# Performance work log

Hardware: AMD Instinct MI355X
Metric: run time of the kernel (lower is better)

The kernel has to match this reference:

```python
import jax, jax.numpy as jnp
import numpy as np

B = 4096
D = 64  # emb_dim, hardcoded in UserEmb/ItemEmb


def setup_inputs() -> dict:
    key = jax.random.key(0)
    ks = jax.random.split(key, 26)
    n = lambda k, shape, s=1.0: jax.random.normal(k, shape, dtype=jnp.float32) * s
    inp = {
        'user_emb': jax.random.randint(ks[0], (B, 4), 0, 6, dtype=jnp.int32),
        'item_emb': jax.random.randint(ks[1], (B, 10242), 0, 2, dtype=jnp.int32),
        'edge_emb': jnp.zeros((B,), dtype=jnp.int32),  # edges_emb has num_embeddings=1
        # UserEmb params
        'gender_tab': n(ks[2], (98, D)),
        'age_tab': n(ks[3], (7, D)),
        'occ_tab': n(ks[4], (21, D)),
        'area_tab': n(ks[5], (3402, D)),
        'user_W': n(ks[6], (4 * D, D), 0.05),  # stored [in,out]
        'user_b': n(ks[7], (D,), 0.05),
        # ItemEmb params
        'rate_tab': n(ks[8], (6, D)),
        'genre_W': n(ks[9], (25, D), 0.05),
        'director_W': n(ks[10], (2186, D), 0.02),
        'actor_W': n(ks[11], (8030, D), 0.01),
        'item_W': n(ks[12], (4 * D, D), 0.05),
        'item_b': n(ks[13], (D,), 0.05),
        # GLNFeat params (torch: randn * 0.5)
        'edges_tab': n(ks[14], (1, D)),
        'uu_w': n(ks[15], (D,), 0.5),
        'ui_w': n(ks[16], (D,), 0.5),
        'iu_w': n(ks[17], (D,), 0.5),
        'ii_w': n(ks[18], (D,), 0.5),
        'edge_W': n(ks[19], (D, D), 0.5),
        'uu_W1': n(ks[20], (D, D), 0.5),
        'ui_W1': n(ks[21], (D, D), 0.5),
        'iu_W1': n(ks[22], (D, D), 0.5),
        'ii_W1': n(ks[23], (D, D), 0.5),
    }
    return inp


def _lrelu(v):
    return jnp.where(v >= 0, v, 0.01 * v)  # nn.LeakyReLU default slope


def reference(user_emb, item_emb, edge_emb, gender_tab, age_tab, occ_tab, area_tab,
              user_W, user_b, rate_tab, genre_W, director_W, actor_W, item_W, item_b,
              edges_tab, uu_w, ui_w, iu_w, ii_w, edge_W, uu_W1, ui_W1, iu_W1, ii_W1):
    a = 0.12
    b = 0.12
    # UserEmb
    u_cat = jnp.concatenate([gender_tab[user_emb[:, 0]], age_tab[user_emb[:, 1]],
                             occ_tab[user_emb[:, 2]], area_tab[user_emb[:, 3]]], axis=1)
    x = (u_cat @ user_W + user_b) * a  # [B, D]
    # ItemEmb: multi-hot fields projected then mean-normalized by count
    genre = item_emb[:, 1:26].astype(jnp.float32)
    director = item_emb[:, 26:2212].astype(jnp.float32)
    actor = item_emb[:, 2212:10242].astype(jnp.float32)
    ge = (genre @ genre_W) / jnp.sum(genre, 1, keepdims=True)
    de = (director @ director_W) / jnp.sum(director, 1, keepdims=True)
    ae = (actor @ actor_W) / jnp.sum(actor, 1, keepdims=True)
    i_cat = jnp.concatenate([rate_tab[item_emb[:, 0]], ge, de, ae], axis=1)
    y = (i_cat @ item_W + item_b) * a  # [B, D]
    edge = edges_tab[edge_emb] * b  # [B, D]

    def outer_mm(u, v, M):
        # stop_gradient(outer(u, v) @ M) == u[:,None] * (v @ M), avoids [B,B]
        return jax.lax.stop_gradient(u[:, None] * (v @ M))

    xe = x * edge
    ye = y * edge
    x_xx = xe @ uu_w      # [B]
    x_xy_x = xe @ ui_w
    x_xy_y = ye @ ui_w
    t1 = outer_mm(x_xx, x_xx, x)
    t2 = outer_mm(x_xy_x, x_xy_y, y)
    x_buy = (_lrelu(t1 @ uu_W1) + _lrelu(t2 @ ui_W1)) / 2
    y_yy = ye @ ii_w
    y_yx_y = ye @ iu_w
    y_yx_x = xe @ iu_w
    t3 = outer_mm(y_yy, y_yy, y)
    t4 = outer_mm(y_yx_y, y_yx_x, x)
    y_buy = (_lrelu(t3 @ ii_W1) + _lrelu(t4 @ iu_W1)) / 2
    new = _lrelu(edge @ edge_W)
    return ((x_buy + x) / 2, (y_buy + y) / 2, (new + edge) / 2)
```

## Files before the change

### kernel.cpp

```cpp
#include <hip/hip_runtime.h>
#include <cstddef>

constexpr int BATCH = 4096;
constexpr int ITEM_COLS = 10242;
constexpr int FBTK = 10304;

constexpr int R_GENDER = 0;
constexpr int R_AGE    = 98;
constexpr int R_OCC    = 105;
constexpr int R_AREA   = 126;
constexpr int R_RATE   = 3528;
constexpr int R_FU     = 3534;

constexpr size_t OFF_FU  = 0;
constexpr size_t OFF_NEW = OFF_FU + (size_t)R_FU * 64;
constexpr size_t OFF_FBT = OFF_NEW + 64;
constexpr size_t OFF_X   = OFF_FBT + (size_t)64 * FBTK / 2;
constexpr size_t OFF_Y   = OFF_X + (size_t)BATCH * 64;
constexpr size_t OFF_P   = OFF_Y + (size_t)BATCH * 64;
constexpr size_t OFF_C   = OFF_P + 9ull * BATCH * 64;
constexpr size_t OFF_SP  = OFF_C + 9ull * BATCH;
constexpr size_t OFF_PB  = OFF_SP + 256ull * 256;
constexpr size_t OFF_SC  = OFF_PB + 4ull * 64;

__device__ const int ASTART[9] = {1, 25, 1113, 2209, 3545, 4881, 6225, 7561, 8897};
__device__ const int VSTART[9] = {1, 26, 1119, 2212, 3550, 4888, 6227, 7565, 8903};
__device__ const int VEND[9]   = {26, 1119, 2212, 3550, 4888, 6227, 7565, 8903, 10242};

typedef __attribute__((ext_vector_type(8))) short bf16x8;
typedef __attribute__((ext_vector_type(4))) float f32x4;

__device__ __forceinline__ float lrelu(float v) { return v >= 0.0f ? v : 0.01f * v; }

__device__ __forceinline__ short bf_trunc(float f) {
    return (short)(__builtin_bit_cast(unsigned, f) >> 16);
}
__device__ __forceinline__ unsigned bf_rne_pair(float lo, float hi) {
    unsigned ul = __builtin_bit_cast(unsigned, lo);
    unsigned uh = __builtin_bit_cast(unsigned, hi);
    ul += 0x7fffu + ((ul >> 16) & 1u);
    uh += 0x7fffu + ((uh >> 16) & 1u);
    return (ul >> 16) | (uh & 0xffff0000u);
}

__global__ __launch_bounds__(256) void k_fuseA(
        const float* __restrict__ gender_tab, const float* __restrict__ age_tab,
        const float* __restrict__ occ_tab, const float* __restrict__ area_tab,
        const float* __restrict__ user_W, const float* __restrict__ rate_tab,
        const float* __restrict__ item_W, const float* __restrict__ edges_tab,
        const float* __restrict__ edge_W, float* __restrict__ Fu, float* __restrict__ NEWt) {
    int t = threadIdx.x;
    int n = t & 63;
    int rb = __builtin_amdgcn_readfirstlane(t >> 6);
    int r = blockIdx.x * 4 + rb;
    if (r > R_FU) return;
    if (r == R_FU) {
        float acc = 0.0f;
#pragma unroll
        for (int k = 0; k < 64; ++k)
            acc = fmaf(edges_tab[k] * 0.12f, edge_W[k * 64 + n], acc);
        NEWt[n] = lrelu(acc);
        return;
    }
    const float* src;
    const float* W;
    if (r < R_AGE)       { src = gender_tab + (size_t)r * 64;            W = user_W;            }
    else if (r < R_OCC)  { src = age_tab    + (size_t)(r - R_AGE) * 64;  W = user_W + 64 * 64;  }
    else if (r < R_AREA) { src = occ_tab    + (size_t)(r - R_OCC) * 64;  W = user_W + 128 * 64; }
    else if (r < R_RATE) { src = area_tab   + (size_t)(r - R_AREA) * 64; W = user_W + 192 * 64; }
    else                 { src = rate_tab   + (size_t)(r - R_RATE) * 64; W = item_W;            }
    float acc = 0.0f;
#pragma unroll
    for (int k = 0; k < 64; ++k)
        acc = fmaf(src[k], W[k * 64 + n], acc);
    Fu[(size_t)r * 64 + n] = acc;
}

__global__ __launch_bounds__(256) void k_fuseT(
        const float* __restrict__ genre_W, const float* __restrict__ director_W,
        const float* __restrict__ actor_W, const float* __restrict__ item_W,
        short* __restrict__ Fbt) {
    const int t = threadIdx.x;
    const int KT0 = blockIdx.x * 64;
    const int n = t & 63;
    const int rb = __builtin_amdgcn_readfirstlane(t >> 6);
    __shared__ float T[64 * 65];
    for (int rl = 0; rl < 16; ++rl) {
        int r = rl * 4 + rb;
        int KT = KT0 + r;
        float acc = 0.0f;
        if (KT < 10241) {
            const float* src;
            const float* W;
            if (KT < 25)        { src = genre_W    + (size_t)KT * 64;          W = item_W + 64 * 64;  }
            else if (KT < 2211) { src = director_W + (size_t)(KT - 25) * 64;   W = item_W + 128 * 64; }
            else                { src = actor_W    + (size_t)(KT - 2211) * 64; W = item_W + 192 * 64; }
#pragma unroll
            for (int k = 0; k < 64; ++k)
                acc = fmaf(src[k], W[k * 64 + n], acc);
        }
        T[r * 65 + n] = acc;
    }
    __syncthreads();
    int n2 = t >> 2, sg = t & 3;
    unsigned dw[8];
#pragma unroll
    for (int d = 0; d < 8; ++d)
        dw[d] = bf_rne_pair(T[(sg * 16 + 2 * d) * 65 + n2], T[(sg * 16 + 2 * d + 1) * 65 + n2]);
    uint4* dst = (uint4*)(Fbt + (size_t)n2 * FBTK + KT0 + sg * 16);
    dst[0] = make_uint4(dw[0], dw[1], dw[2], dw[3]);
    dst[1] = make_uint4(dw[4], dw[5], dw[6], dw[7]);
}

__global__ __launch_bounds__(256) void k_item(const int* __restrict__ item,
                                              const short* __restrict__ Fbt,
                                              float* __restrict__ P, float* __restrict__ C) {
    const int ch = blockIdx.y;
    const int astart = ASTART[ch], vs = VSTART[ch], ve = VEND[ch];
    const int len = ve - astart;
    const int KT0 = astart - 1;
    const int m0 = blockIdx.x * 64;
    const int t = threadIdx.x;
    const int lane = t & 63;
    const int w = __builtin_amdgcn_readfirstlane(t >> 6);
    const int q = lane >> 4, r16 = lane & 15;

    __shared__ short As[64 * 136];
    __shared__ short Bs[64 * 136];

    f32x4 acc[5];
#pragma unroll
    for (int s = 0; s < 5; ++s) acc[s] = (f32x4){0.f, 0.f, 0.f, 0.f};

    short o = (r16 == 0) ? (short)0x3f80 : (short)0;
    bf16x8 ones = {o, o, o, o, o, o, o, o};

    for (int kb = 0; kb < len; kb += 128) {
        __syncthreads();
        const int c0 = astart + kb;
        if (c0 >= vs && c0 + 128 <= ve) {
#pragma unroll
            for (int it = 0; it < 32; ++it) {
                int f = it * 256 + t;
                int r = f >> 7, cc = f & 127;
                int v = item[(size_t)(m0 + r) * ITEM_COLS + c0 + cc];
                As[r * 136 + cc] = bf_trunc((float)v);
            }
        } else {
#pragma unroll
            for (int it = 0; it < 32; ++it) {
                int f = it * 256 + t;
                int r = f >> 7, cc = f & 127;
                int c = c0 + cc;
                int v = (c >= vs && c < ve) ? item[(size_t)(m0 + r) * ITEM_COLS + c] : 0;
                As[r * 136 + cc] = bf_trunc((float)v);
            }
        }
        {
            int nB = t >> 2, pt = t & 3;
            const short* fb = Fbt + (size_t)nB * FBTK + KT0 + kb;
#pragma unroll
            for (int p = 0; p < 4; ++p) {
                int off = (p * 4 + pt) * 8;
                *(uint4*)(Bs + nB * 136 + off) = *(const uint4*)(fb + off);
            }
        }
        __syncthreads();
#pragma unroll
        for (int kt = 0; kt < 4; ++kt) {
            bf16x8 a = *(const bf16x8*)(As + (w * 16 + r16) * 136 + kt * 32 + q * 8);
#pragma unroll
            for (int s = 0; s < 4; ++s) {
                bf16x8 b = *(const bf16x8*)(Bs + (s * 16 + r16) * 136 + kt * 32 + q * 8);
                acc[s] = __builtin_amdgcn_mfma_f32_16x16x32_bf16(a, b, acc[s], 0, 0, 0);
            }
            acc[4] = __builtin_amdgcn_mfma_f32_16x16x32_bf16(a, ones, acc[4], 0, 0, 0);
        }
    }
    const size_t pb = (size_t)ch * BATCH + m0 + w * 16 + q * 4;
#pragma unroll
    for (int reg = 0; reg < 4; ++reg) {
        float* pr = P + (pb + reg) * 64 + r16;
        pr[0] = acc[0][reg];
        pr[16] = acc[1][reg];
        pr[32] = acc[2][reg];
        pr[48] = acc[3][reg];
    }
    if (r16 == 0) {
#pragma unroll
        for (int reg = 0; reg < 4; ++reg)
            C[(size_t)ch * BATCH + m0 + w * 16 + q * 4 + reg] = acc[4][reg];
    }
}

__device__ __forceinline__ float wred(float v) {
#pragma unroll
    for (int m = 1; m < 64; m <<= 1) v += __shfl_xor(v, m, 64);
    return v;
}

__global__ __launch_bounds__(256) void k_mid(const int* __restrict__ item, const int* __restrict__ edge_emb,
                                             const int* __restrict__ user_emb,
                                             const float* __restrict__ Fu, const float* __restrict__ user_b,
                                             const float* __restrict__ P, const float* __restrict__ C,
                                             const float* __restrict__ item_b, const float* __restrict__ edges_tab,
                                             const float* __restrict__ uu_w, const float* __restrict__ ui_w,
                                             const float* __restrict__ iu_w, const float* __restrict__ ii_w,
                                             float* __restrict__ X, float* __restrict__ Y,
                                             float* __restrict__ SC, float* __restrict__ SP) {
    const int t = threadIdx.x;
    const int n = t & 63;
    const int wv = __builtin_amdgcn_readfirstlane(t >> 6);
    const float uuw = uu_w[n], uiw = ui_w[n], iuw = iu_w[n], iiw = ii_w[n];
    const float ib = item_b[n], ub = user_b[n];
    const size_t cs = (size_t)BATCH * 64;
    float s1 = 0.0f, s2 = 0.0f, s3 = 0.0f, s4 = 0.0f;

    for (int i = 0; i < 4; ++i) {
        int b = blockIdx.x * 16 + wv * 4 + i;
        const int* ue = user_emb + (size_t)b * 4;
        float x = (Fu[(size_t)(R_GENDER + ue[0]) * 64 + n]
                 + Fu[(size_t)(R_AGE    + ue[1]) * 64 + n]
                 + Fu[(size_t)(R_OCC    + ue[2]) * 64 + n]
                 + Fu[(size_t)(R_AREA   + ue[3]) * 64 + n] + ub) * 0.12f;
        X[(size_t)b * 64 + n] = x;
        int ri = item[(size_t)b * ITEM_COLS];
        size_t base = (size_t)b * 64 + n;
        float sg = P[base];
        float sd = P[base + cs] + P[base + 2 * cs];
        float sa = P[base + 3 * cs] + P[base + 4 * cs] + P[base + 5 * cs]
                 + P[base + 6 * cs] + P[base + 7 * cs] + P[base + 8 * cs];
        float cg = C[b];
        float cd = C[BATCH + b] + C[2 * BATCH + b];
        float ca = C[3 * BATCH + b] + C[4 * BATCH + b] + C[5 * BATCH + b]
                 + C[6 * BATCH + b] + C[7 * BATCH + b] + C[8 * BATCH + b];
        float y = (Fu[(size_t)(R_RATE + ri) * 64 + n] + sg / cg + sd / cd + sa / ca + ib) * 0.12f;
        Y[(size_t)b * 64 + n] = y;
        float e = edges_tab[(size_t)edge_emb[b] * 64 + n] * 0.12f;
        float xe = x * e, ye = y * e;
        float r1 = wred(xe * uuw);
        float r2 = wred(xe * uiw);
        float r3 = wred(xe * iuw);
        float r4 = wred(ye * uiw);
        float r5 = wred(ye * iiw);
        float r6 = wred(ye * iuw);
        if (n == 0) {
            SC[b] = r1; SC[BATCH + b] = r2; SC[2 * BATCH + b] = r5; SC[3 * BATCH + b] = r6;
        }
        s1 = fmaf(r1, x, s1);
        s2 = fmaf(r4, y, s2);
        s3 = fmaf(r5, y, s3);
        s4 = fmaf(r3, x, s4);
    }
    __shared__ float sp[4][4][64];
    sp[wv][0][n] = s1; sp[wv][1][n] = s2; sp[wv][2][n] = s3; sp[wv][3][n] = s4;
    __syncthreads();
    int i2 = t >> 6;
    float v = sp[0][i2][n] + sp[1][i2][n] + sp[2][i2][n] + sp[3][i2][n];
    SP[(size_t)blockIdx.x * 256 + t] = v;
}

__global__ __launch_bounds__(1024) void k_red(const float* __restrict__ SP,
                                              const float* __restrict__ uu_W1, const float* __restrict__ ui_W1,
                                              const float* __restrict__ iu_W1, const float* __restrict__ ii_W1,
                                              float* __restrict__ PB) {
    int t = threadIdx.x;
    int sub = t >> 8, i = (t >> 6) & 3, n = t & 63;
    float s = 0.0f;
    for (int wb = sub * 64; wb < sub * 64 + 64; ++wb)
        s += SP[(size_t)wb * 256 + i * 64 + n];
    __shared__ float red[4][4][64];
    red[sub][i][n] = s;
    __syncthreads();
    float sv = red[0][i][n] + red[1][i][n] + red[2][i][n] + red[3][i][n];
    __shared__ float sl[4][64];
    if (t < 256) sl[i][n] = sv;
    __syncthreads();
    if (t < 256) {
        const float* W1 = (i == 0) ? uu_W1 : (i == 1) ? ui_W1 : (i == 2) ? ii_W1 : iu_W1;
        float p = 0.0f;
#pragma unroll
        for (int k = 0; k < 64; ++k) p = fmaf(sl[i][k], W1[k * 64 + n], p);
        PB[i * 64 + n] = p;
    }
}

__global__ __launch_bounds__(256) void k_out(const float* __restrict__ X, const float* __restrict__ Y,
                                             const float* __restrict__ SC, const float* __restrict__ PB,
                                             const float* __restrict__ NEWt, const float* __restrict__ edges_tab,
                                             const int* __restrict__ edge_emb, float* __restrict__ out) {
    int t = threadIdx.x;
    int b = blockIdx.x * 4 + (t >> 6);
    int n = t & 63;
    float xx = SC[b], xyx = SC[BATCH + b], yy = SC[2 * BATCH + b], yxy = SC[3 * BATCH + b];
    float p1 = PB[n], p2 = PB[64 + n], p3 = PB[128 + n], p4 = PB[192 + n];
    float x = X[(size_t)b * 64 + n], y = Y[(size_t)b * 64 + n];
    float o1 = ((lrelu(xx * p1) + lrelu(xyx * p2)) * 0.5f + x) * 0.5f;
    float o2 = ((lrelu(yy * p3) + lrelu(yxy * p4)) * 0.5f + y) * 0.5f;
    int ei = edge_emb[b];
    float e = edges_tab[(size_t)ei * 64 + n] * 0.12f;
    float o3 = (NEWt[n] + e) * 0.5f;
    out[(size_t)b * 64 + n] = o1;
    out[((size_t)BATCH + b) * 64 + n] = o2;
    out[((size_t)2 * BATCH + b) * 64 + n] = o3;
}

extern "C" void kernel_launch(void* const* d_in, const int* in_sizes, int n_in,
                              void* d_out, int out_size, void* d_ws, size_t ws_size,
                              hipStream_t stream) {
    (void)in_sizes; (void)n_in; (void)out_size; (void)ws_size;
    const int*   user_emb   = (const int*)  d_in[0];
    const int*   item_emb   = (const int*)  d_in[1];
    const int*   edge_emb   = (const int*)  d_in[2];
    const float* gender_tab = (const float*)d_in[3];
    const float* age_tab    = (const float*)d_in[4];
    const float* occ_tab    = (const float*)d_in[5];
    const float* area_tab   = (const float*)d_in[6];
    const float* user_W     = (const float*)d_in[7];
    const float* user_b     = (const float*)d_in[8];
    const float* rate_tab   = (const float*)d_in[9];
    const float* genre_W    = (const float*)d_in[10];
    const float* director_W = (const float*)d_in[11];
    const float* actor_W    = (const float*)d_in[12];
    const float* item_W     = (const float*)d_in[13];
    const float* item_b     = (const float*)d_in[14];
    const float* edges_tab  = (const float*)d_in[15];
    const float* uu_w       = (const float*)d_in[16];
    const float* ui_w       = (const float*)d_in[17];
    const float* iu_w       = (const float*)d_in[18];
    const float* ii_w       = (const float*)d_in[19];
    const float* edge_W     = (const float*)d_in[20];
    const float* uu_W1      = (const float*)d_in[21];
    const float* ui_W1      = (const float*)d_in[22];
    const float* iu_W1      = (const float*)d_in[23];
    const float* ii_W1      = (const float*)d_in[24];

    float* ws   = (float*)d_ws;
    float* Fu   = ws + OFF_FU;
    float* NEWt = ws + OFF_NEW;
    short* Fbt  = (short*)(ws + OFF_FBT);
    float* X    = ws + OFF_X;
    float* Y    = ws + OFF_Y;
    float* P    = ws + OFF_P;
    float* C    = ws + OFF_C;
    float* SP   = ws + OFF_SP;
    float* PB   = ws + OFF_PB;
    float* SC   = ws + OFF_SC;
    float* out  = (float*)d_out;

    hipLaunchKernelGGL(k_fuseA, dim3(884), dim3(256), 0, stream,
                       gender_tab, age_tab, occ_tab, area_tab, user_W, rate_tab,
                       item_W, edges_tab, edge_W, Fu, NEWt);
    hipLaunchKernelGGL(k_fuseT, dim3(FBTK / 64), dim3(256), 0, stream,
                       genre_W, director_W, actor_W, item_W, Fbt);
    hipLaunchKernelGGL(k_item, dim3(BATCH / 64, 9), dim3(256), 0, stream, item_emb, Fbt, P, C);
    hipLaunchKernelGGL(k_mid, dim3(BATCH / 16), dim3(256), 0, stream,
                       item_emb, edge_emb, user_emb, Fu, user_b, P, C, item_b, edges_tab,
                       uu_w, ui_w, iu_w, ii_w, X, Y, SC, SP);
    hipLaunchKernelGGL(k_red, dim3(1), dim3(1024), 0, stream, SP, uu_W1, ui_W1, iu_W1, ii_W1, PB);
    hipLaunchKernelGGL(k_out, dim3(BATCH / 4), dim3(256), 0, stream,
                       X, Y, SC, PB, NEWt, edges_tab, edge_emb, out);
}
```

Baseline: 357.7 us.

## Fuse table-fusion kernels and align item chunk loads with padded per-chunk weight layout

Merges the two weight-fusion kernels into one launch and reorganizes the fused bf16 item weight matrix into per-chunk padded blocks whose start columns are 8-aligned. This lets the item GEMM kernel load the int32 multi-hot matrix with aligned int2 vector loads and convert to bf16 ones with a select instead of int-to-float conversion. Out-of-range columns are zeroed in the weights, and the count column is masked only on edge tiles. It adds padding work and per-tile masking logic in exchange for cheaper, wider global loads of the dominant input.

```diff
diff --git a/kernel.cpp b/kernel.cpp
--- a/kernel.cpp
+++ b/kernel.cpp
@@ -3,7 +3,6 @@
 
 constexpr int BATCH = 4096;
 constexpr int ITEM_COLS = 10242;
-constexpr int FBTK = 10304;
 
 constexpr int R_GENDER = 0;
 constexpr int R_AGE    = 98;
@@ -12,10 +11,18 @@
 constexpr int R_RATE   = 3528;
 constexpr int R_FU     = 3534;
 
+__device__ const int CBASE[9]  = {0, 24, 1112, 2208, 3544, 4880, 6224, 7560, 8896};
+__device__ const int VSTART[9] = {1, 26, 1119, 2212, 3550, 4888, 6227, 7565, 8903};
+__device__ const int VEND[9]   = {26, 1119, 2212, 3550, 4888, 6227, 7565, 8903, 10242};
+__device__ const int CUM[10]   = {0, 128, 1280, 2432, 3840, 5248, 6656, 8064, 9472, 10880};
+constexpr int FB2COLS = 10880;
+constexpr int NFUSEA = 884;
+constexpr int NFUSET = FB2COLS / 64;
+
 constexpr size_t OFF_FU  = 0;
 constexpr size_t OFF_NEW = OFF_FU + (size_t)R_FU * 64;
 constexpr size_t OFF_FBT = OFF_NEW + 64;
-constexpr size_t OFF_X   = OFF_FBT + (size_t)64 * FBTK / 2;
+constexpr size_t OFF_X   = OFF_FBT + (size_t)64 * FB2COLS / 2;
 constexpr size_t OFF_Y   = OFF_X + (size_t)BATCH * 64;
 constexpr size_t OFF_P   = OFF_Y + (size_t)BATCH * 64;
 constexpr size_t OFF_C   = OFF_P + 9ull * BATCH * 64;
@@ -23,18 +30,11 @@
 constexpr size_t OFF_PB  = OFF_SP + 256ull * 256;
 constexpr size_t OFF_SC  = OFF_PB + 4ull * 64;
 
-__device__ const int ASTART[9] = {1, 25, 1113, 2209, 3545, 4881, 6225, 7561, 8897};
-__device__ const int VSTART[9] = {1, 26, 1119, 2212, 3550, 4888, 6227, 7565, 8903};
-__device__ const int VEND[9]   = {26, 1119, 2212, 3550, 4888, 6227, 7565, 8903, 10242};
-
 typedef __attribute__((ext_vector_type(8))) short bf16x8;
 typedef __attribute__((ext_vector_type(4))) float f32x4;
 
 __device__ __forceinline__ float lrelu(float v) { return v >= 0.0f ? v : 0.01f * v; }
 
-__device__ __forceinline__ short bf_trunc(float f) {
-    return (short)(__builtin_bit_cast(unsigned, f) >> 16);
-}
 __device__ __forceinline__ unsigned bf_rne_pair(float lo, float hi) {
     unsigned ul = __builtin_bit_cast(unsigned, lo);
     unsigned uh = __builtin_bit_cast(unsigned, hi);
@@ -43,58 +43,63 @@
     return (ul >> 16) | (uh & 0xffff0000u);
 }
 
-__global__ __launch_bounds__(256) void k_fuseA(
+__global__ __launch_bounds__(256) void k_fuse(
         const float* __restrict__ gender_tab, const float* __restrict__ age_tab,
         const float* __restrict__ occ_tab, const float* __restrict__ area_tab,
         const float* __restrict__ user_W, const float* __restrict__ rate_tab,
         const float* __restrict__ item_W, const float* __restrict__ edges_tab,
-        const float* __restrict__ edge_W, float* __restrict__ Fu, float* __restrict__ NEWt) {
-    int t = threadIdx.x;
-    int n = t & 63;
-    int rb = __builtin_amdgcn_readfirstlane(t >> 6);
-    int r = blockIdx.x * 4 + rb;
-    if (r > R_FU) return;
-    if (r == R_FU) {
-        float acc = 0.0f;
-#pragma unroll
-        for (int k = 0; k < 64; ++k)
-            acc = fmaf(edges_tab[k] * 0.12f, edge_W[k * 64 + n], acc);
-        NEWt[n] = lrelu(acc);
-        return;
-    }
-    const float* src;
-    const float* W;
-    if (r < R_AGE)       { src = gender_tab + (size_t)r * 64;            W = user_W;            }
-    else if (r < R_OCC)  { src = age_tab    + (size_t)(r - R_AGE) * 64;  W = user_W + 64 * 64;  }
-    else if (r < R_AREA) { src = occ_tab    + (size_t)(r - R_OCC) * 64;  W = user_W + 128 * 64; }
-    else if (r < R_RATE) { src = area_tab   + (size_t)(r - R_AREA) * 64; W = user_W + 192 * 64; }
-    else                 { src = rate_tab   + (size_t)(r - R_RATE) * 64; W = item_W;            }
-    float acc = 0.0f;
-#pragma unroll
-    for (int k = 0; k < 64; ++k)
-        acc = fmaf(src[k], W[k * 64 + n], acc);
-    Fu[(size_t)r * 64 + n] = acc;
-}
-
-__global__ __launch_bounds__(256) void k_fuseT(
-        const float* __restrict__ genre_W, const float* __restrict__ director_W,
-        const float* __restrict__ actor_W, const float* __restrict__ item_W,
-        short* __restrict__ Fbt) {
+        const float* __restrict__ edge_W, const float* __restrict__ genre_W,
+        const float* __restrict__ director_W, const float* __restrict__ actor_W,
+        float* __restrict__ Fu, float* __restrict__ NEWt, short* __restrict__ Fbt2) {
     const int t = threadIdx.x;
-    const int KT0 = blockIdx.x * 64;
     const int n = t & 63;
     const int rb = __builtin_amdgcn_readfirstlane(t >> 6);
     __shared__ float T[64 * 65];
+    const int blk = blockIdx.x;
+
+    if (blk < NFUSEA) {
+        int r = blk * 4 + rb;
+        if (r > R_FU) return;
+        if (r == R_FU) {
+            float acc = 0.0f;
+#pragma unroll
+            for (int k = 0; k < 64; ++k)
+                acc = fmaf(edges_tab[k] * 0.12f, edge_W[k * 64 + n], acc);
+            NEWt[n] = lrelu(acc);
+            return;
+        }
+        const float* src;
+        const float* W;
+        if (r < R_AGE)       { src = gender_tab + (size_t)r * 64;            W = user_W;            }
+        else if (r < R_OCC)  { src = age_tab    + (size_t)(r - R_AGE) * 64;  W = user_W + 64 * 64;  }
+        else if (r < R_AREA) { src = occ_tab    + (size_t)(r - R_OCC) * 64;  W = user_W + 128 * 64; }
+        else if (r < R_RATE) { src = area_tab   + (size_t)(r - R_AREA) * 64; W = user_W + 192 * 64; }
+        else                 { src = rate_tab   + (size_t)(r - R_RATE) * 64; W = item_W;            }
+        float acc = 0.0f;
+#pragma unroll
+        for (int k = 0; k < 64; ++k)
+            acc = fmaf(src[k], W[k * 64 + n], acc);
+        Fu[(size_t)r * 64 + n] = acc;
+        return;
+    }
+
+    const int g0 = (blk - NFUSEA) * 64;
+    int ch = 0;
+    while (g0 >= CUM[ch + 1]) ++ch;
+    const int kk0 = g0 - CUM[ch];
+    const int lenp = CUM[ch + 1] - CUM[ch];
+    const int cb = CBASE[ch], vs = VSTART[ch], ve = VEND[ch];
+
     for (int rl = 0; rl < 16; ++rl) {
         int r = rl * 4 + rb;
-        int KT = KT0 + r;
+        int c = cb + kk0 + r;
         float acc = 0.0f;
-        if (KT < 10241) {
+        if (c >= vs && c < ve) {
             const float* src;
             const float* W;
-            if (KT < 25)        { src = genre_W    + (size_t)KT * 64;          W = item_W + 64 * 64;  }
-            else if (KT < 2211) { src = director_W + (size_t)(KT - 25) * 64;   W = item_W + 128 * 64; }
-            else                { src = actor_W    + (size_t)(KT - 2211) * 64; W = item_W + 192 * 64; }
+            if (c < 26)        { src = genre_W    + (size_t)(c - 1) * 64;    W = item_W + 64 * 64;  }
+            else if (c < 2212) { src = director_W + (size_t)(c - 26) * 64;   W = item_W + 128 * 64; }
+            else               { src = actor_W    + (size_t)(c - 2212) * 64; W = item_W + 192 * 64; }
 #pragma unroll
             for (int k = 0; k < 64; ++k)
                 acc = fmaf(src[k], W[k * 64 + n], acc);
@@ -107,18 +112,20 @@
 #pragma unroll
     for (int d = 0; d < 8; ++d)
         dw[d] = bf_rne_pair(T[(sg * 16 + 2 * d) * 65 + n2], T[(sg * 16 + 2 * d + 1) * 65 + n2]);
-    uint4* dst = (uint4*)(Fbt + (size_t)n2 * FBTK + KT0 + sg * 16);
+    uint4* dst = (uint4*)(Fbt2 + (size_t)64 * CUM[ch] + (size_t)n2 * lenp + kk0 + sg * 16);
     dst[0] = make_uint4(dw[0], dw[1], dw[2], dw[3]);
     dst[1] = make_uint4(dw[4], dw[5], dw[6], dw[7]);
 }
 
 __global__ __launch_bounds__(256) void k_item(const int* __restrict__ item,
-                                              const short* __restrict__ Fbt,
+                                              const short* __restrict__ Fbt2,
                                               float* __restrict__ P, float* __restrict__ C) {
     const int ch = blockIdx.y;
-    const int astart = ASTART[ch], vs = VSTART[ch], ve = VEND[ch];
-    const int len = ve - astart;
-    const int KT0 = astart - 1;
+    const int cb = CBASE[ch], vs = VSTART[ch], ve = VEND[ch];
+    const int lo = vs - cb;
+    const int hi = ve - cb;
+    const int lenp = CUM[ch + 1] - CUM[ch];
+    const short* FB = Fbt2 + (size_t)64 * CUM[ch];
     const int m0 = blockIdx.x * 64;
     const int t = threadIdx.x;
     const int lane = t & 63;
@@ -132,19 +139,20 @@
 #pragma unroll
     for (int s = 0; s < 5; ++s) acc[s] = (f32x4){0.f, 0.f, 0.f, 0.f};
 
-    short o = (r16 == 0) ? (short)0x3f80 : (short)0;
-    bf16x8 ones = {o, o, o, o, o, o, o, o};
-
-    for (int kb = 0; kb < len; kb += 128) {
+    const short o = (r16 == 0) ? (short)0x3f80 : (short)0;
+    const bf16x8 ones = {o, o, o, o, o, o, o, o};
+
+    for (int kb = 0; kb < hi; kb += 128) {
         __syncthreads();
-        const int c0 = astart + kb;
-        if (c0 >= vs && c0 + 128 <= ve) {
-#pragma unroll
-            for (int it = 0; it < 32; ++it) {
+        const int c0 = cb + kb;
+        if (c0 + 128 <= ITEM_COLS) {
+#pragma unroll
+            for (int it = 0; it < 16; ++it) {
                 int f = it * 256 + t;
-                int r = f >> 7, cc = f & 127;
-                int v = item[(size_t)(m0 + r) * ITEM_COLS + c0 + cc];
-                As[r * 136 + cc] = bf_trunc((float)v);
+                int r = f >> 6, c2 = f & 63;
+                int2 v = *(const int2*)(item + (size_t)(m0 + r) * ITEM_COLS + c0 + c2 * 2);
+                unsigned d = (v.x ? 0x3f80u : 0u) | (v.y ? 0x3f800000u : 0u);
+                *(unsigned*)(As + r * 136 + c2 * 2) = d;
             }
         } else {
 #pragma unroll
@@ -152,13 +160,13 @@
                 int f = it * 256 + t;
                 int r = f >> 7, cc = f & 127;
                 int c = c0 + cc;
-                int v = (c >= vs && c < ve) ? item[(size_t)(m0 + r) * ITEM_COLS + c] : 0;
-                As[r * 136 + cc] = bf_trunc((float)v);
+                int v = (c < ITEM_COLS) ? item[(size_t)(m0 + r) * ITEM_COLS + c] : 0;
+                As[r * 136 + cc] = v ? (short)0x3f80 : (short)0;
             }
         }
         {
             int nB = t >> 2, pt = t & 3;
-            const short* fb = Fbt + (size_t)nB * FBTK + KT0 + kb;
+            const short* fb = FB + (size_t)nB * lenp + kb;
 #pragma unroll
             for (int p = 0; p < 4; ++p) {
                 int off = (p * 4 + pt) * 8;
@@ -166,15 +174,24 @@
             }
         }
         __syncthreads();
+        const bool edge = (kb < lo) || (kb + 128 > hi);
 #pragma unroll
         for (int kt = 0; kt < 4; ++kt) {
             bf16x8 a = *(const bf16x8*)(As + (w * 16 + r16) * 136 + kt * 32 + q * 8);
+            bf16x8 ov = ones;
+            if (edge) {
+#pragma unroll
+                for (int j = 0; j < 8; ++j) {
+                    int ks = kb + kt * 32 + q * 8 + j;
+                    ov[j] = (ks >= lo && ks < hi) ? o : (short)0;
+                }
+            }
 #pragma unroll
             for (int s = 0; s < 4; ++s) {
                 bf16x8 b = *(const bf16x8*)(Bs + (s * 16 + r16) * 136 + kt * 32 + q * 8);
                 acc[s] = __builtin_amdgcn_mfma_f32_16x16x32_bf16(a, b, acc[s], 0, 0, 0);
             }
-            acc[4] = __builtin_amdgcn_mfma_f32_16x16x32_bf16(a, ones, acc[4], 0, 0, 0);
+            acc[4] = __builtin_amdgcn_mfma_f32_16x16x32_bf16(a, ov, acc[4], 0, 0, 0);
         }
     }
     const size_t pb = (size_t)ch * BATCH + m0 + w * 16 + q * 4;
@@ -338,7 +355,7 @@
     float* ws   = (float*)d_ws;
     float* Fu   = ws + OFF_FU;
     float* NEWt = ws + OFF_NEW;
-    short* Fbt  = (short*)(ws + OFF_FBT);
+    short* Fbt2 = (short*)(ws + OFF_FBT);
     float* X    = ws + OFF_X;
     float* Y    = ws + OFF_Y;
     float* P    = ws + OFF_P;
@@ -348,12 +365,11 @@
     float* SC   = ws + OFF_SC;
     float* out  = (float*)d_out;
 
-    hipLaunchKernelGGL(k_fuseA, dim3(884), dim3(256), 0, stream,
+    hipLaunchKernelGGL(k_fuse, dim3(NFUSEA + NFUSET), dim3(256), 0, stream,
                        gender_tab, age_tab, occ_tab, area_tab, user_W, rate_tab,
-                       item_W, edges_tab, edge_W, Fu, NEWt);
-    hipLaunchKernelGGL(k_fuseT, dim3(FBTK / 64), dim3(256), 0, stream,
-                       genre_W, director_W, actor_W, item_W, Fbt);
-    hipLaunchKernelGGL(k_item, dim3(BATCH / 64, 9), dim3(256), 0, stream, item_emb, Fbt, P, C);
+                       item_W, edges_tab, edge_W, genre_W, director_W, actor_W,
+                       Fu, NEWt, Fbt2);
+    hipLaunchKernelGGL(k_item, dim3(BATCH / 64, 9), dim3(256), 0, stream, item_emb, Fbt2, P, C);
     hipLaunchKernelGGL(k_mid, dim3(BATCH / 16), dim3(256), 0, stream,
                        item_emb, edge_emb, user_emb, Fu, user_b, P, C, item_b, edges_tab,
                        uu_w, ui_w, iu_w, ii_w, X, Y, SC, SP);
```

Result: faster. 348.8 us (-2.5%).
